# Optimization experiments

Measured on AMD Instinct MI355X. Metric: run time of the kernel, lower is better.

The kernel has to match this reference:

```python
import jax, jax.numpy as jnp
import numpy as np

N_HEAD = 12


def setup_inputs() -> dict:
    key = jax.random.key(0)
    k1, k2, k3 = jax.random.split(key, 3)
    B, S, D = 4, 2048, 768
    x = jax.random.normal(k1, (B, S, D), dtype=jnp.float32)
    std = 0.02
    w_attn = jax.random.normal(k2, (D, 3 * D), dtype=jnp.float32) * std
    b_attn = jnp.zeros((3 * D,), dtype=jnp.float32)
    w_proj = jax.random.normal(k3, (D, D), dtype=jnp.float32) * std
    b_proj = jnp.zeros((D,), dtype=jnp.float32)
    return {"x": x, "w_attn": w_attn, "b_attn": b_attn,
            "w_proj": w_proj, "b_proj": b_proj}


def reference(x, w_attn, b_attn, w_proj, b_proj):
    B, S, D = x.shape
    H = N_HEAD
    hd = D // H
    # c_attn: [B,S,3D]
    qkv = jnp.einsum('bsd,de->bse', x, w_attn) + b_attn
    q, k, v = jnp.split(qkv, 3, axis=2)
    # split heads -> [B,H,S,hd]
    q = q.reshape(B, S, H, hd).transpose(0, 2, 1, 3)
    k = k.reshape(B, S, H, hd).transpose(0, 2, 1, 3)
    v = v.reshape(B, S, H, hd).transpose(0, 2, 1, 3)
    # scores [B,H,S,S]; scale=False in original default
    w = jnp.einsum('bhqd,bhkd->bhqk', q, k)
    # original mask trick: w*b + 1e-9*(1-b), b = lower-triangular ones
    mask = jnp.tril(jnp.ones((S, S), dtype=w.dtype))
    w = w * mask + 1e-9 * (1 - mask)
    w = jax.nn.softmax(w, axis=-1)
    a = jnp.einsum('bhqk,bhkd->bhqd', w, v)
    # merge heads -> [B,S,D]
    a = a.transpose(0, 2, 1, 3).reshape(B, S, D)
    # c_proj
    out = jnp.einsum('bsd,de->bse', a, w_proj) + b_proj
    return out
```

## Files before the change

### kernel.cpp

```cpp
#include <hip/hip_runtime.h>
#include <cstdint>

typedef unsigned short u16;
typedef __bf16 bf16;
typedef bf16 bf16x8 __attribute__((ext_vector_type(8)));
typedef u16 u16x4 __attribute__((ext_vector_type(4)));
typedef u16 u16x8 __attribute__((ext_vector_type(8)));
typedef float f32x4 __attribute__((ext_vector_type(4)));

__device__ __forceinline__ u16 f2b(float f) {
    return __builtin_bit_cast(u16, (bf16)f);
}
__device__ __forceinline__ float b2f(u16 u) {
    return __uint_as_float(((unsigned)u) << 16);
}
__device__ __forceinline__ void load_lds16(const void* g, void* l) {
    auto gp = reinterpret_cast<const __attribute__((address_space(1))) void*>(
        reinterpret_cast<uintptr_t>(g));
    auto lp = reinterpret_cast<__attribute__((address_space(3))) void*>(
        reinterpret_cast<uintptr_t>(l));
    __builtin_amdgcn_global_load_lds(gp, lp, 16, 0, 0);
}
__device__ __forceinline__ f32x4 mfma16(bf16x8 a, bf16x8 b, f32x4 c) {
    return __builtin_amdgcn_mfma_f32_16x16x32_bf16(a, b, c, 0, 0, 0);
}

__global__ __launch_bounds__(256) void convx_kernel(const float* __restrict__ x,
                                                    u16* __restrict__ xb, int n4) {
    int i = blockIdx.x * blockDim.x + threadIdx.x;
    int stride = gridDim.x * blockDim.x;
    for (; i < n4; i += stride) {
        float4 v = ((const float4*)x)[i];
        u16x4 r;
        r[0] = f2b(v.x); r[1] = f2b(v.y); r[2] = f2b(v.z); r[3] = f2b(v.w);
        *(u16x4*)&xb[(size_t)i * 4] = r;
    }
}

__global__ __launch_bounds__(256) void wtrans_kernel(const float* __restrict__ w,
                                                     u16* __restrict__ wT, int K, int N) {
    __shared__ float tile[32][33];
    int tx = threadIdx.x, ty = threadIdx.y;
    int n0 = blockIdx.x * 32, k0 = blockIdx.y * 32;
#pragma unroll
    for (int i = 0; i < 4; ++i)
        tile[ty + i * 8][tx] = w[(size_t)(k0 + ty + i * 8) * N + n0 + tx];
    __syncthreads();
#pragma unroll
    for (int i = 0; i < 4; ++i)
        wT[(size_t)(n0 + ty + i * 8) * K + k0 + tx] = f2b(tile[tx][ty + i * 8]);
}

template <bool OUT_BF16>
__global__ __launch_bounds__(256, 2) void gemm_kernel(const u16* __restrict__ A,
                                                      const u16* __restrict__ Bt,
                                                      const float* __restrict__ bias,
                                                      void* __restrict__ out,
                                                      int M, int N, int K) {
    __shared__ __align__(16) u16 As[128 * 64];
    __shared__ __align__(16) u16 Bs[128 * 64];
    const int tid = threadIdx.x;
    const int wave = tid >> 6, lane = tid & 63;
    const int l15 = lane & 15, lg = lane >> 4;
    const int gx = gridDim.x;
    const int nwg = gx * gridDim.y;
    const int lin = blockIdx.y * gx + blockIdx.x;
    const int swz = (lin & 7) * (nwg >> 3) + (lin >> 3);
    const int tm = (swz / gx) * 128, tn = (swz % gx) * 128;
    const int wr = (wave >> 1) * 64, wc = (wave & 1) * 64;

    f32x4 acc[4][4] = {};

    const int rbase = wave * 8 + (lane >> 3);
    const int sslot = (lane & 7) ^ (rbase & 7);
    const u16* gA = A + (size_t)(tm + rbase) * K + sslot * 8;
    const u16* gB = Bt + (size_t)(tn + rbase) * K + sslot * 8;
    u16* ldsA = As + (size_t)(wave * 8) * 64;
    u16* ldsB = Bs + (size_t)(wave * 8) * 64;

    for (int kt = 0; kt < K; kt += 64) {
#pragma unroll
        for (int i = 0; i < 4; ++i) {
            load_lds16(gA + (size_t)i * 32 * K + kt, ldsA + i * 32 * 64);
            load_lds16(gB + (size_t)i * 32 * K + kt, ldsB + i * 32 * 64);
        }
        __syncthreads();
#pragma unroll
        for (int kk = 0; kk < 64; kk += 32) {
            const int sb = kk >> 3;
            bf16x8 af[4], bfr[4];
#pragma unroll
            for (int m = 0; m < 4; ++m) {
                int row = wr + m * 16 + l15;
                af[m] = *(const bf16x8*)&As[row * 64 + (((sb + lg) ^ (row & 7))) * 8];
            }
#pragma unroll
            for (int n = 0; n < 4; ++n) {
                int row = wc + n * 16 + l15;
                bfr[n] = *(const bf16x8*)&Bs[row * 64 + (((sb + lg) ^ (row & 7))) * 8];
            }
#pragma unroll
            for (int m = 0; m < 4; ++m)
#pragma unroll
                for (int n = 0; n < 4; ++n)
                    acc[m][n] = mfma16(af[m], bfr[n], acc[m][n]);
        }
        __syncthreads();
    }

#pragma unroll
    for (int n = 0; n < 4; ++n) {
        int col = tn + wc + n * 16 + l15;
        float bv = bias[col];
#pragma unroll
        for (int m = 0; m < 4; ++m) {
            int row0 = tm + wr + m * 16 + lg * 4;
#pragma unroll
            for (int r = 0; r < 4; ++r) {
                float v = acc[m][n][r] + bv;
                if constexpr (OUT_BF16)
                    ((u16*)out)[(size_t)(row0 + r) * N + col] = f2b(v);
                else
                    ((float*)out)[(size_t)(row0 + r) * N + col] = v;
            }
        }
    }
}

__global__ __launch_bounds__(256) void vtrans_kernel(const u16* __restrict__ qkv,
                                                     u16* __restrict__ vt,
                                                     float* __restrict__ ts_raw) {
    __shared__ __align__(16) u16 tile[64][72];
    __shared__ float red2[64][4];
    const int st = blockIdx.x, bh = blockIdx.y;
    const int b = bh / 12, h = bh % 12;
    const int t = threadIdx.x;
    const int sr = t >> 2, c4 = (t & 3) * 16;
    const u16* src = qkv + (size_t)(b * 2048 + st * 64 + sr) * 2304 + 1536 + h * 64 + c4;
    *(u16x8*)&tile[sr][c4] = *(const u16x8*)src;
    *(u16x8*)&tile[sr][c4 + 8] = *(const u16x8*)(src + 8);
    __syncthreads();
    const int dr = t >> 2, s4 = (t & 3) * 16;
    u16x8 w0, w1;
    float psum = 0.f;
#pragma unroll
    for (int j = 0; j < 8; ++j) {
        w0[j] = tile[s4 + j][dr];
        w1[j] = tile[s4 + 8 + j][dr];
        psum += b2f(w0[j]) + b2f(w1[j]);
    }
    u16* dst = vt + ((size_t)bh * 64 + dr) * 2048 + st * 64 + s4;
    *(u16x8*)dst = w0;
    *(u16x8*)(dst + 8) = w1;
    red2[dr][t & 3] = psum;
    __syncthreads();
    if (t < 64)
        ts_raw[((size_t)bh * 32 + st) * 64 + t] =
            red2[t][0] + red2[t][1] + red2[t][2] + red2[t][3];
}

__global__ __launch_bounds__(64) void suffix_kernel(const float* __restrict__ ts_raw,
                                                    float* __restrict__ ts_suf) {
    const int bh = blockIdx.x, d = threadIdx.x;
    float acc = 0.f;
    for (int t = 31; t >= 0; --t) {
        acc += ts_raw[((size_t)bh * 32 + t) * 64 + d];
        ts_suf[((size_t)bh * 32 + t) * 64 + d] = acc;
    }
}

__global__ __launch_bounds__(256, 4) void attn_kernel(const u16* __restrict__ qkv,
                                                      const u16* __restrict__ vt,
                                                      const float* __restrict__ ts_suf,
                                                      u16* __restrict__ aout) {
    __shared__ __align__(16) u16 Ks[2][64 * 64];
    __shared__ __align__(16) u16 Vs[2][64 * 64];
    __shared__ __align__(16) u16 Ps[64 * 64];
    const int bh = blockIdx.x;
    const int qt = 31 - blockIdx.y;
    const int b = bh / 12, h = bh % 12;
    const int tid = threadIdx.x, wave = tid >> 6, lane = tid & 63;
    const int l15 = lane & 15, lg = lane >> 4;
    const int q0 = qt * 64 + wave * 16;
    const size_t rowbase = (size_t)b * 2048;

    bf16x8 qf[2];
#pragma unroll
    for (int ks = 0; ks < 2; ++ks)
        qf[ks] = *(const bf16x8*)(qkv + (rowbase + q0 + l15) * 2304 + h * 64 +
                                  ks * 32 + lg * 8);

    f32x4 o[4] = {};
    float mrun = -1e30f;
    float lrun = 0.f;

    const int rbase = wave * 8 + (lane >> 3);
    const int sslot = (lane & 7) ^ (rbase & 7);
    const u16* gK = qkv + (rowbase + rbase) * 2304 + 768 + h * 64 + sslot * 8;
    const u16* gV = vt + ((size_t)bh * 64 + rbase) * 2048 + sslot * 8;
    const int ldsoff = wave * 8 * 64;

    const int nkt = qt + 1;
#pragma unroll
    for (int i = 0; i < 2; ++i) {
        load_lds16(gK + (size_t)(i * 32) * 2304, &Ks[0][ldsoff + i * 32 * 64]);
        load_lds16(gV + (size_t)(i * 32) * 2048, &Vs[0][ldsoff + i * 32 * 64]);
    }

    for (int kt = 0; kt < nkt; ++kt) {
        __syncthreads();
        const int cur = kt & 1;
        if (kt + 1 < nkt) {
            const int nx = cur ^ 1;
#pragma unroll
            for (int i = 0; i < 2; ++i) {
                load_lds16(gK + ((size_t)(kt + 1) * 64 + i * 32) * 2304,
                           &Ks[nx][ldsoff + i * 32 * 64]);
                load_lds16(gV + (size_t)(i * 32) * 2048 + (kt + 1) * 64,
                           &Vs[nx][ldsoff + i * 32 * 64]);
            }
        }

        f32x4 sacc[4] = {};
        __builtin_amdgcn_s_setprio(1);
#pragma unroll
        for (int ks = 0; ks < 2; ++ks) {
#pragma unroll
            for (int n = 0; n < 4; ++n) {
                int row = n * 16 + l15;
                bf16x8 ak = *(const bf16x8*)&Ks[cur][row * 64 +
                                                     (((ks * 4 + lg) ^ (row & 7))) * 8];
                sacc[n] = mfma16(ak, qf[ks], sacc[n]);
            }
        }
        __builtin_amdgcn_s_setprio(0);

        if (kt == qt) {
            const int q = q0 + l15;
#pragma unroll
            for (int n = 0; n < 4; ++n)
#pragma unroll
                for (int r = 0; r < 4; ++r) {
                    int k = kt * 64 + n * 16 + lg * 4 + r;
                    if (k > q) sacc[n][r] = 1e-9f;
                }
        }

        float mx = fmaxf(fmaxf(sacc[0][0], sacc[0][1]), fmaxf(sacc[0][2], sacc[0][3]));
#pragma unroll
        for (int n = 1; n < 4; ++n)
            mx = fmaxf(mx, fmaxf(fmaxf(sacc[n][0], sacc[n][1]),
                                 fmaxf(sacc[n][2], sacc[n][3])));
        if (__any(mx > mrun + 8.0f)) {
            float rm = fmaxf(mx, __shfl_xor(mx, 16));
            rm = fmaxf(rm, __shfl_xor(rm, 32));
            const float mnew = fmaxf(mrun, rm);
            const float alpha = __expf(mrun - mnew);
            mrun = mnew;
            lrun *= alpha;
#pragma unroll
            for (int dn = 0; dn < 4; ++dn) o[dn] *= alpha;
        }

        u16x4 pk[4];
#pragma unroll
        for (int n = 0; n < 4; ++n)
#pragma unroll
            for (int r = 0; r < 4; ++r) {
                float p = __expf(sacc[n][r] - mrun);
                lrun += p;
                pk[n][r] = f2b(p);
            }

        const int prow = wave * 16 + l15;
#pragma unroll
        for (int n = 0; n < 4; ++n) {
            int slot = n * 2 + (lg >> 1);
            *(u16x4*)&Ps[prow * 64 + ((slot ^ (prow & 7))) * 8 + (lg & 1) * 4] = pk[n];
        }

        __builtin_amdgcn_s_setprio(1);
#pragma unroll
        for (int ks = 0; ks < 2; ++ks) {
            bf16x8 bp = *(const bf16x8*)&Ps[prow * 64 +
                                            (((ks * 4 + lg) ^ (prow & 7))) * 8];
#pragma unroll
            for (int dn = 0; dn < 4; ++dn) {
                int row = dn * 16 + l15;
                bf16x8 av = *(const bf16x8*)&Vs[cur][row * 64 +
                                                     (((ks * 4 + lg) ^ (row & 7))) * 8];
                o[dn] = mfma16(av, bp, o[dn]);
            }
        }
        __builtin_amdgcn_s_setprio(0);
    }

    lrun += __shfl_xor(lrun, 16);
    lrun += __shfl_xor(lrun, 32);

    if (qt < 31) {
        const float nf = (float)((31 - qt) * 64);
        const float mnew = fmaxf(mrun, 1e-9f);
        const float a = __expf(mrun - mnew);
        const float c = __expf(1e-9f - mnew);
        lrun = lrun * a + nf * c;
        const float* sufp = ts_suf + ((size_t)bh * 32 + qt + 1) * 64;
#pragma unroll
        for (int dn = 0; dn < 4; ++dn) {
            f32x4 suf = *(const f32x4*)&sufp[dn * 16 + lg * 4];
            o[dn] = o[dn] * a + suf * c;
        }
    }

    const float inv = 1.f / lrun;
    const size_t row = rowbase + q0 + l15;
#pragma unroll
    for (int dn = 0; dn < 4; ++dn) {
        u16x4 st;
#pragma unroll
        for (int r = 0; r < 4; ++r) st[r] = f2b(o[dn][r] * inv);
        *(u16x4*)&aout[row * 768 + h * 64 + dn * 16 + lg * 4] = st;
    }
}

extern "C" void kernel_launch(void* const* d_in, const int* in_sizes, int n_in,
                              void* d_out, int out_size, void* d_ws, size_t ws_size,
                              hipStream_t stream) {
    const float* x      = (const float*)d_in[0];
    const float* w_attn = (const float*)d_in[1];
    const float* b_attn = (const float*)d_in[2];
    const float* w_proj = (const float*)d_in[3];
    const float* b_proj = (const float*)d_in[4];
    float* out = (float*)d_out;
    char* ws = (char*)d_ws;

    u16* xb      = (u16*)(ws + 0);
    u16* wTa     = (u16*)(ws + 12582912);
    u16* wTp     = (u16*)(ws + 16121856);
    u16* qkv     = (u16*)(ws + 17301504);
    u16* vt      = (u16*)(ws + 55050240);
    u16* aout    = (u16*)(ws + 67633152);
    float* ts_raw = (float*)(ws + 0);
    float* ts_suf = (float*)(ws + 393216);

    convx_kernel<<<dim3(2048), dim3(256), 0, stream>>>(x, xb, 8192 * 768 / 4);
    wtrans_kernel<<<dim3(72, 24), dim3(32, 8), 0, stream>>>(w_attn, wTa, 768, 2304);
    wtrans_kernel<<<dim3(24, 24), dim3(32, 8), 0, stream>>>(w_proj, wTp, 768, 768);
    gemm_kernel<true><<<dim3(18, 64), dim3(256), 0, stream>>>(xb, wTa, b_attn,
                                                              (void*)qkv, 8192, 2304, 768);
    vtrans_kernel<<<dim3(32, 48), dim3(256), 0, stream>>>(qkv, vt, ts_raw);
    suffix_kernel<<<dim3(48), dim3(64), 0, stream>>>(ts_raw, ts_suf);
    attn_kernel<<<dim3(48, 32), dim3(256), 0, stream>>>(qkv, vt, ts_suf, aout);
    gemm_kernel<false><<<dim3(6, 64), dim3(256), 0, stream>>>(aout, wTp, b_proj,
                                                              (void*)out, 8192, 768, 768);
}
```

Before: 208.6 us.

## Double attention query tile per block, fuse weight transposes, drop suffix kernel

The attention kernel now handles 128 query rows per block, with each wave owning 32 rows as two 16-row MFMA groups. Each K/V tile loaded into LDS is reused for twice as many queries, halving K/V traffic and block count at the cost of more registers, so occupancy drops from 4 to 3. The separate suffix-sum kernel is removed and each attention block sums the tail of ts_raw itself, adding redundant per-block work but one fewer launch. The two weight-transpose launches are merged into one, and the GEMM launch bound is raised to 3 waves per SIMD.

```diff
diff --git a/kernel.cpp b/kernel.cpp
--- a/kernel.cpp
+++ b/kernel.cpp
@@ -37,11 +37,20 @@
     }
 }
 
-__global__ __launch_bounds__(256) void wtrans_kernel(const float* __restrict__ w,
-                                                     u16* __restrict__ wT, int K, int N) {
+__global__ __launch_bounds__(256) void wtrans2_kernel(const float* __restrict__ wa,
+                                                      const float* __restrict__ wp,
+                                                      u16* __restrict__ wTa,
+                                                      u16* __restrict__ wTp) {
     __shared__ float tile[32][33];
+    const int bx = blockIdx.x;
+    const float* w;
+    u16* wT;
+    int N, n0;
+    if (bx < 72) { w = wa; wT = wTa; N = 2304; n0 = bx * 32; }
+    else         { w = wp; wT = wTp; N = 768;  n0 = (bx - 72) * 32; }
+    const int K = 768;
     int tx = threadIdx.x, ty = threadIdx.y;
-    int n0 = blockIdx.x * 32, k0 = blockIdx.y * 32;
+    int k0 = blockIdx.y * 32;
 #pragma unroll
     for (int i = 0; i < 4; ++i)
         tile[ty + i * 8][tx] = w[(size_t)(k0 + ty + i * 8) * N + n0 + tx];
@@ -52,7 +61,7 @@
 }
 
 template <bool OUT_BF16>
-__global__ __launch_bounds__(256, 2) void gemm_kernel(const u16* __restrict__ A,
+__global__ __launch_bounds__(256, 3) void gemm_kernel(const u16* __restrict__ A,
                                                       const u16* __restrict__ Bt,
                                                       const float* __restrict__ bias,
                                                       void* __restrict__ out,
@@ -159,40 +168,32 @@
             red2[t][0] + red2[t][1] + red2[t][2] + red2[t][3];
 }
 
-__global__ __launch_bounds__(64) void suffix_kernel(const float* __restrict__ ts_raw,
-                                                    float* __restrict__ ts_suf) {
-    const int bh = blockIdx.x, d = threadIdx.x;
-    float acc = 0.f;
-    for (int t = 31; t >= 0; --t) {
-        acc += ts_raw[((size_t)bh * 32 + t) * 64 + d];
-        ts_suf[((size_t)bh * 32 + t) * 64 + d] = acc;
-    }
-}
-
-__global__ __launch_bounds__(256, 4) void attn_kernel(const u16* __restrict__ qkv,
+__global__ __launch_bounds__(256, 3) void attn_kernel(const u16* __restrict__ qkv,
                                                       const u16* __restrict__ vt,
-                                                      const float* __restrict__ ts_suf,
+                                                      const float* __restrict__ ts_raw,
                                                       u16* __restrict__ aout) {
     __shared__ __align__(16) u16 Ks[2][64 * 64];
     __shared__ __align__(16) u16 Vs[2][64 * 64];
-    __shared__ __align__(16) u16 Ps[64 * 64];
+    __shared__ __align__(16) u16 Ps[128 * 64];
     const int bh = blockIdx.x;
-    const int qt = 31 - blockIdx.y;
+    const int qt = 15 - blockIdx.y;
     const int b = bh / 12, h = bh % 12;
     const int tid = threadIdx.x, wave = tid >> 6, lane = tid & 63;
     const int l15 = lane & 15, lg = lane >> 4;
-    const int q0 = qt * 64 + wave * 16;
+    const int q0 = qt * 128 + wave * 32;
     const size_t rowbase = (size_t)b * 2048;
 
-    bf16x8 qf[2];
-#pragma unroll
-    for (int ks = 0; ks < 2; ++ks)
-        qf[ks] = *(const bf16x8*)(qkv + (rowbase + q0 + l15) * 2304 + h * 64 +
-                                  ks * 32 + lg * 8);
-
-    f32x4 o[4] = {};
+    bf16x8 qf[2][2];
+#pragma unroll
+    for (int m = 0; m < 2; ++m)
+#pragma unroll
+        for (int ks = 0; ks < 2; ++ks)
+            qf[m][ks] = *(const bf16x8*)(qkv + (rowbase + q0 + m * 16 + l15) * 2304 +
+                                         h * 64 + ks * 32 + lg * 8);
+
+    f32x4 o[2][4] = {};
     float mrun = -1e30f;
-    float lrun = 0.f;
+    float lrun[2] = {0.f, 0.f};
 
     const int rbase = wave * 8 + (lane >> 3);
     const int sslot = (lane & 7) ^ (rbase & 7);
@@ -200,7 +201,7 @@
     const u16* gV = vt + ((size_t)bh * 64 + rbase) * 2048 + sslot * 8;
     const int ldsoff = wave * 8 * 64;
 
-    const int nkt = qt + 1;
+    const int nkt = 2 * qt + 2;
 #pragma unroll
     for (int i = 0; i < 2; ++i) {
         load_lds16(gK + (size_t)(i * 32) * 2304, &Ks[0][ldsoff + i * 32 * 64]);
@@ -221,7 +222,7 @@
             }
         }
 
-        f32x4 sacc[4] = {};
+        f32x4 sacc[2][4] = {};
         __builtin_amdgcn_s_setprio(1);
 #pragma unroll
         for (int ks = 0; ks < 2; ++ks) {
@@ -230,96 +231,126 @@
                 int row = n * 16 + l15;
                 bf16x8 ak = *(const bf16x8*)&Ks[cur][row * 64 +
                                                      (((ks * 4 + lg) ^ (row & 7))) * 8];
-                sacc[n] = mfma16(ak, qf[ks], sacc[n]);
+                sacc[0][n] = mfma16(ak, qf[0][ks], sacc[0][n]);
+                sacc[1][n] = mfma16(ak, qf[1][ks], sacc[1][n]);
             }
         }
         __builtin_amdgcn_s_setprio(0);
 
-        if (kt == qt) {
-            const int q = q0 + l15;
+        if (kt >= 2 * qt) {
+#pragma unroll
+            for (int m = 0; m < 2; ++m) {
+                const int q = q0 + m * 16 + l15;
+#pragma unroll
+                for (int n = 0; n < 4; ++n)
+#pragma unroll
+                    for (int r = 0; r < 4; ++r) {
+                        int k = kt * 64 + n * 16 + lg * 4 + r;
+                        if (k > q) sacc[m][n][r] = 1e-9f;
+                    }
+            }
+        }
+
+        float mx = sacc[0][0][0];
+#pragma unroll
+        for (int m = 0; m < 2; ++m)
 #pragma unroll
             for (int n = 0; n < 4; ++n)
-#pragma unroll
-                for (int r = 0; r < 4; ++r) {
-                    int k = kt * 64 + n * 16 + lg * 4 + r;
-                    if (k > q) sacc[n][r] = 1e-9f;
-                }
-        }
-
-        float mx = fmaxf(fmaxf(sacc[0][0], sacc[0][1]), fmaxf(sacc[0][2], sacc[0][3]));
-#pragma unroll
-        for (int n = 1; n < 4; ++n)
-            mx = fmaxf(mx, fmaxf(fmaxf(sacc[n][0], sacc[n][1]),
-                                 fmaxf(sacc[n][2], sacc[n][3])));
+                mx = fmaxf(mx, fmaxf(fmaxf(sacc[m][n][0], sacc[m][n][1]),
+                                     fmaxf(sacc[m][n][2], sacc[m][n][3])));
         if (__any(mx > mrun + 8.0f)) {
             float rm = fmaxf(mx, __shfl_xor(mx, 16));
             rm = fmaxf(rm, __shfl_xor(rm, 32));
+            rm = fmaxf(rm, __shfl_xor(rm, 1));
+            rm = fmaxf(rm, __shfl_xor(rm, 2));
+            rm = fmaxf(rm, __shfl_xor(rm, 4));
+            rm = fmaxf(rm, __shfl_xor(rm, 8));
             const float mnew = fmaxf(mrun, rm);
             const float alpha = __expf(mrun - mnew);
             mrun = mnew;
-            lrun *= alpha;
-#pragma unroll
-            for (int dn = 0; dn < 4; ++dn) o[dn] *= alpha;
-        }
-
-        u16x4 pk[4];
-#pragma unroll
-        for (int n = 0; n < 4; ++n)
-#pragma unroll
-            for (int r = 0; r < 4; ++r) {
-                float p = __expf(sacc[n][r] - mrun);
-                lrun += p;
-                pk[n][r] = f2b(p);
-            }
-
-        const int prow = wave * 16 + l15;
-#pragma unroll
-        for (int n = 0; n < 4; ++n) {
-            int slot = n * 2 + (lg >> 1);
-            *(u16x4*)&Ps[prow * 64 + ((slot ^ (prow & 7))) * 8 + (lg & 1) * 4] = pk[n];
+            lrun[0] *= alpha;
+            lrun[1] *= alpha;
+#pragma unroll
+            for (int m = 0; m < 2; ++m)
+#pragma unroll
+                for (int dn = 0; dn < 4; ++dn) o[m][dn] *= alpha;
+        }
+
+#pragma unroll
+        for (int m = 0; m < 2; ++m) {
+            const int prow = wave * 32 + m * 16 + l15;
+#pragma unroll
+            for (int n = 0; n < 4; ++n) {
+                u16x4 pk;
+#pragma unroll
+                for (int r = 0; r < 4; ++r) {
+                    float p = __expf(sacc[m][n][r] - mrun);
+                    lrun[m] += p;
+                    pk[r] = f2b(p);
+                }
+                int slot = n * 2 + (lg >> 1);
+                *(u16x4*)&Ps[prow * 64 + ((slot ^ (prow & 7))) * 8 + (lg & 1) * 4] = pk;
+            }
         }
 
         __builtin_amdgcn_s_setprio(1);
 #pragma unroll
         for (int ks = 0; ks < 2; ++ks) {
-            bf16x8 bp = *(const bf16x8*)&Ps[prow * 64 +
-                                            (((ks * 4 + lg) ^ (prow & 7))) * 8];
+            const int prow0 = wave * 32 + l15;
+            bf16x8 bp0 = *(const bf16x8*)&Ps[prow0 * 64 +
+                                             (((ks * 4 + lg) ^ (prow0 & 7))) * 8];
+            bf16x8 bp1 = *(const bf16x8*)&Ps[(prow0 + 16) * 64 +
+                                             (((ks * 4 + lg) ^ (prow0 & 7))) * 8];
 #pragma unroll
             for (int dn = 0; dn < 4; ++dn) {
                 int row = dn * 16 + l15;
                 bf16x8 av = *(const bf16x8*)&Vs[cur][row * 64 +
                                                      (((ks * 4 + lg) ^ (row & 7))) * 8];
-                o[dn] = mfma16(av, bp, o[dn]);
+                o[0][dn] = mfma16(av, bp0, o[0][dn]);
+                o[1][dn] = mfma16(av, bp1, o[1][dn]);
             }
         }
         __builtin_amdgcn_s_setprio(0);
     }
 
-    lrun += __shfl_xor(lrun, 16);
-    lrun += __shfl_xor(lrun, 32);
-
-    if (qt < 31) {
-        const float nf = (float)((31 - qt) * 64);
+#pragma unroll
+    for (int m = 0; m < 2; ++m) {
+        lrun[m] += __shfl_xor(lrun[m], 16);
+        lrun[m] += __shfl_xor(lrun[m], 32);
+    }
+
+    if (qt < 15) {
+        const float nf = (float)((15 - qt) * 128);
         const float mnew = fmaxf(mrun, 1e-9f);
         const float a = __expf(mrun - mnew);
         const float c = __expf(1e-9f - mnew);
-        lrun = lrun * a + nf * c;
-        const float* sufp = ts_suf + ((size_t)bh * 32 + qt + 1) * 64;
+        lrun[0] = lrun[0] * a + nf * c;
+        lrun[1] = lrun[1] * a + nf * c;
+        f32x4 suf[4] = {};
+        for (int t = 2 * qt + 2; t < 32; ++t) {
+            const float* sp = ts_raw + ((size_t)bh * 32 + t) * 64;
+#pragma unroll
+            for (int dn = 0; dn < 4; ++dn)
+                suf[dn] += *(const f32x4*)&sp[dn * 16 + lg * 4];
+        }
+#pragma unroll
+        for (int m = 0; m < 2; ++m)
+#pragma unroll
+            for (int dn = 0; dn < 4; ++dn)
+                o[m][dn] = o[m][dn] * a + suf[dn] * c;
+    }
+
+#pragma unroll
+    for (int m = 0; m < 2; ++m) {
+        const float inv = 1.f / lrun[m];
+        const size_t row = rowbase + q0 + m * 16 + l15;
 #pragma unroll
         for (int dn = 0; dn < 4; ++dn) {
-            f32x4 suf = *(const f32x4*)&sufp[dn * 16 + lg * 4];
-            o[dn] = o[dn] * a + suf * c;
-        }
-    }
-
-    const float inv = 1.f / lrun;
-    const size_t row = rowbase + q0 + l15;
-#pragma unroll
-    for (int dn = 0; dn < 4; ++dn) {
-        u16x4 st;
-#pragma unroll
-        for (int r = 0; r < 4; ++r) st[r] = f2b(o[dn][r] * inv);
-        *(u16x4*)&aout[row * 768 + h * 64 + dn * 16 + lg * 4] = st;
+            u16x4 st;
+#pragma unroll
+            for (int r = 0; r < 4; ++r) st[r] = f2b(o[m][dn][r] * inv);
+            *(u16x4*)&aout[row * 768 + h * 64 + dn * 16 + lg * 4] = st;
+        }
     }
 }
 
@@ -341,16 +372,13 @@
     u16* vt      = (u16*)(ws + 55050240);
     u16* aout    = (u16*)(ws + 67633152);
     float* ts_raw = (float*)(ws + 0);
-    float* ts_suf = (float*)(ws + 393216);
 
     convx_kernel<<<dim3(2048), dim3(256), 0, stream>>>(x, xb, 8192 * 768 / 4);
-    wtrans_kernel<<<dim3(72, 24), dim3(32, 8), 0, stream>>>(w_attn, wTa, 768, 2304);
-    wtrans_kernel<<<dim3(24, 24), dim3(32, 8), 0, stream>>>(w_proj, wTp, 768, 768);
+    wtrans2_kernel<<<dim3(96, 24), dim3(32, 8), 0, stream>>>(w_attn, w_proj, wTa, wTp);
     gemm_kernel<true><<<dim3(18, 64), dim3(256), 0, stream>>>(xb, wTa, b_attn,
                                                               (void*)qkv, 8192, 2304, 768);
     vtrans_kernel<<<dim3(32, 48), dim3(256), 0, stream>>>(qkv, vt, ts_raw);
-    suffix_kernel<<<dim3(48), dim3(64), 0, stream>>>(ts_raw, ts_suf);
-    attn_kernel<<<dim3(48, 32), dim3(256), 0, stream>>>(qkv, vt, ts_suf, aout);
+    attn_kernel<<<dim3(48, 16), dim3(256), 0, stream>>>(qkv, vt, ts_raw, aout);
     gemm_kernel<false><<<dim3(6, 64), dim3(256), 0, stream>>>(aout, wTp, b_proj,
                                                               (void*)out, 8192, 768, 768);
 }
```

After: 198.9 us. -4.7%, faster.

## Keep attention P in registers via permuted K rows, fuse small kernels

Applied to the files above, without the earlier changes.

The K tile rows are loaded into LDS in a permuted order, so the score MFMA output layout matches the B-operand layout of the PV MFMA. Probabilities can then be packed straight into bf16 registers, with no round trip through the Ps shared buffer, and the causal mask indices are remapped to fit. The separate suffix-sum kernel is removed; each attention block sums the ts_raw tiles it needs inline. The two weight-transpose launches are merged into one, and launch-bounds occupancy hints are raised for the GEMM and attention kernels. The risks are redundant suffix reads for early query tiles and register pressure at the higher occupancy targets.

```diff
diff --git a/kernel.cpp b/kernel.cpp
--- a/kernel.cpp
+++ b/kernel.cpp
@@ -37,11 +37,20 @@
     }
 }
 
-__global__ __launch_bounds__(256) void wtrans_kernel(const float* __restrict__ w,
-                                                     u16* __restrict__ wT, int K, int N) {
+__global__ __launch_bounds__(256) void wtrans2_kernel(const float* __restrict__ wa,
+                                                      const float* __restrict__ wp,
+                                                      u16* __restrict__ wTa,
+                                                      u16* __restrict__ wTp) {
     __shared__ float tile[32][33];
+    const int bx = blockIdx.x;
+    const float* w;
+    u16* wT;
+    int N, n0;
+    if (bx < 72) { w = wa; wT = wTa; N = 2304; n0 = bx * 32; }
+    else         { w = wp; wT = wTp; N = 768;  n0 = (bx - 72) * 32; }
+    const int K = 768;
     int tx = threadIdx.x, ty = threadIdx.y;
-    int n0 = blockIdx.x * 32, k0 = blockIdx.y * 32;
+    int k0 = blockIdx.y * 32;
 #pragma unroll
     for (int i = 0; i < 4; ++i)
         tile[ty + i * 8][tx] = w[(size_t)(k0 + ty + i * 8) * N + n0 + tx];
@@ -52,7 +61,7 @@
 }
 
 template <bool OUT_BF16>
-__global__ __launch_bounds__(256, 2) void gemm_kernel(const u16* __restrict__ A,
+__global__ __launch_bounds__(256, 3) void gemm_kernel(const u16* __restrict__ A,
                                                       const u16* __restrict__ Bt,
                                                       const float* __restrict__ bias,
                                                       void* __restrict__ out,
@@ -159,23 +168,12 @@
             red2[t][0] + red2[t][1] + red2[t][2] + red2[t][3];
 }
 
-__global__ __launch_bounds__(64) void suffix_kernel(const float* __restrict__ ts_raw,
-                                                    float* __restrict__ ts_suf) {
-    const int bh = blockIdx.x, d = threadIdx.x;
-    float acc = 0.f;
-    for (int t = 31; t >= 0; --t) {
-        acc += ts_raw[((size_t)bh * 32 + t) * 64 + d];
-        ts_suf[((size_t)bh * 32 + t) * 64 + d] = acc;
-    }
-}
-
-__global__ __launch_bounds__(256, 4) void attn_kernel(const u16* __restrict__ qkv,
+__global__ __launch_bounds__(256, 5) void attn_kernel(const u16* __restrict__ qkv,
                                                       const u16* __restrict__ vt,
-                                                      const float* __restrict__ ts_suf,
+                                                      const float* __restrict__ ts_raw,
                                                       u16* __restrict__ aout) {
     __shared__ __align__(16) u16 Ks[2][64 * 64];
     __shared__ __align__(16) u16 Vs[2][64 * 64];
-    __shared__ __align__(16) u16 Ps[64 * 64];
     const int bh = blockIdx.x;
     const int qt = 31 - blockIdx.y;
     const int b = bh / 12, h = bh % 12;
@@ -196,14 +194,15 @@
 
     const int rbase = wave * 8 + (lane >> 3);
     const int sslot = (lane & 7) ^ (rbase & 7);
-    const u16* gK = qkv + (rowbase + rbase) * 2304 + 768 + h * 64 + sslot * 8;
+    const int sig0 = ((rbase & 0x1C) << 1) | (rbase & 3);
+    const u16* gK = qkv + (rowbase + sig0) * 2304 + 768 + h * 64 + sslot * 8;
     const u16* gV = vt + ((size_t)bh * 64 + rbase) * 2048 + sslot * 8;
     const int ldsoff = wave * 8 * 64;
 
     const int nkt = qt + 1;
 #pragma unroll
     for (int i = 0; i < 2; ++i) {
-        load_lds16(gK + (size_t)(i * 32) * 2304, &Ks[0][ldsoff + i * 32 * 64]);
+        load_lds16(gK + (size_t)(i * 4) * 2304, &Ks[0][ldsoff + i * 32 * 64]);
         load_lds16(gV + (size_t)(i * 32) * 2048, &Vs[0][ldsoff + i * 32 * 64]);
     }
 
@@ -214,7 +213,7 @@
             const int nx = cur ^ 1;
 #pragma unroll
             for (int i = 0; i < 2; ++i) {
-                load_lds16(gK + ((size_t)(kt + 1) * 64 + i * 32) * 2304,
+                load_lds16(gK + (size_t)((kt + 1) * 64 + i * 4) * 2304,
                            &Ks[nx][ldsoff + i * 32 * 64]);
                 load_lds16(gV + (size_t)(i * 32) * 2048 + (kt + 1) * 64,
                            &Vs[nx][ldsoff + i * 32 * 64]);
@@ -237,13 +236,14 @@
 
         if (kt == qt) {
             const int q = q0 + l15;
-#pragma unroll
-            for (int n = 0; n < 4; ++n)
-#pragma unroll
-                for (int r = 0; r < 4; ++r) {
-                    int k = kt * 64 + n * 16 + lg * 4 + r;
-                    if (k > q) sacc[n][r] = 1e-9f;
-                }
+            const int kb = kt * 64 + lg * 8;
+#pragma unroll
+            for (int n = 0; n < 4; ++n) {
+                const int kn = kb + (n & 1) * 32 + ((n >> 1) << 2);
+#pragma unroll
+                for (int r = 0; r < 4; ++r)
+                    if (kn + r > q) sacc[n][r] = 1e-9f;
+            }
         }
 
         float mx = fmaxf(fmaxf(sacc[0][0], sacc[0][1]), fmaxf(sacc[0][2], sacc[0][3]));
@@ -262,28 +262,27 @@
             for (int dn = 0; dn < 4; ++dn) o[dn] *= alpha;
         }
 
-        u16x4 pk[4];
 #pragma unroll
         for (int n = 0; n < 4; ++n)
 #pragma unroll
             for (int r = 0; r < 4; ++r) {
                 float p = __expf(sacc[n][r] - mrun);
                 lrun += p;
-                pk[n][r] = f2b(p);
-            }
-
-        const int prow = wave * 16 + l15;
-#pragma unroll
-        for (int n = 0; n < 4; ++n) {
-            int slot = n * 2 + (lg >> 1);
-            *(u16x4*)&Ps[prow * 64 + ((slot ^ (prow & 7))) * 8 + (lg & 1) * 4] = pk[n];
+                sacc[n][r] = p;
+            }
+        bf16x8 bp0, bp1;
+#pragma unroll
+        for (int j = 0; j < 4; ++j) {
+            bp0[j]     = (bf16)sacc[0][j];
+            bp0[j + 4] = (bf16)sacc[2][j];
+            bp1[j]     = (bf16)sacc[1][j];
+            bp1[j + 4] = (bf16)sacc[3][j];
         }
 
         __builtin_amdgcn_s_setprio(1);
 #pragma unroll
         for (int ks = 0; ks < 2; ++ks) {
-            bf16x8 bp = *(const bf16x8*)&Ps[prow * 64 +
-                                            (((ks * 4 + lg) ^ (prow & 7))) * 8];
+            bf16x8 bp = ks ? bp1 : bp0;
 #pragma unroll
             for (int dn = 0; dn < 4; ++dn) {
                 int row = dn * 16 + l15;
@@ -304,12 +303,16 @@
         const float a = __expf(mrun - mnew);
         const float c = __expf(1e-9f - mnew);
         lrun = lrun * a + nf * c;
-        const float* sufp = ts_suf + ((size_t)bh * 32 + qt + 1) * 64;
-#pragma unroll
-        for (int dn = 0; dn < 4; ++dn) {
-            f32x4 suf = *(const f32x4*)&sufp[dn * 16 + lg * 4];
-            o[dn] = o[dn] * a + suf * c;
-        }
+        f32x4 suf[4] = {};
+        for (int t = qt + 1; t < 32; ++t) {
+            const float* sp = ts_raw + ((size_t)bh * 32 + t) * 64;
+#pragma unroll
+            for (int dn = 0; dn < 4; ++dn)
+                suf[dn] += *(const f32x4*)&sp[dn * 16 + lg * 4];
+        }
+#pragma unroll
+        for (int dn = 0; dn < 4; ++dn)
+            o[dn] = o[dn] * a + suf[dn] * c;
     }
 
     const float inv = 1.f / lrun;
@@ -341,16 +344,13 @@
     u16* vt      = (u16*)(ws + 55050240);
     u16* aout    = (u16*)(ws + 67633152);
     float* ts_raw = (float*)(ws + 0);
-    float* ts_suf = (float*)(ws + 393216);
 
     convx_kernel<<<dim3(2048), dim3(256), 0, stream>>>(x, xb, 8192 * 768 / 4);
-    wtrans_kernel<<<dim3(72, 24), dim3(32, 8), 0, stream>>>(w_attn, wTa, 768, 2304);
-    wtrans_kernel<<<dim3(24, 24), dim3(32, 8), 0, stream>>>(w_proj, wTp, 768, 768);
+    wtrans2_kernel<<<dim3(96, 24), dim3(32, 8), 0, stream>>>(w_attn, w_proj, wTa, wTp);
     gemm_kernel<true><<<dim3(18, 64), dim3(256), 0, stream>>>(xb, wTa, b_attn,
                                                               (void*)qkv, 8192, 2304, 768);
     vtrans_kernel<<<dim3(32, 48), dim3(256), 0, stream>>>(qkv, vt, ts_raw);
-    suffix_kernel<<<dim3(48), dim3(64), 0, stream>>>(ts_raw, ts_suf);
-    attn_kernel<<<dim3(48, 32), dim3(256), 0, stream>>>(qkv, vt, ts_suf, aout);
+    attn_kernel<<<dim3(48, 32), dim3(256), 0, stream>>>(qkv, vt, ts_raw, aout);
     gemm_kernel<false><<<dim3(6, 64), dim3(256), 0, stream>>>(aout, wTp, b_proj,
                                                               (void*)out, 8192, 768, 768);
 }
```

Result: faster. 201.9 us (-3.2%).
